# Kernel optimization log

Hardware: AMD Instinct MI355X
Metric: run time of the kernel (lower is better)

The kernel has to match this reference:

```python
import jax, jax.numpy as jnp
import numpy as np

B, D, N, L, M = 32, 64, 128, 192, 32  # batch, channels, nodes, seq_len, modes
LH = L // 2 + 1  # rfft length = 97


def setup_inputs() -> dict:
    key = jax.random.key(0)
    k1, k2, k3 = jax.random.split(key, 3)
    scale = 1.0 / (D * D)  # 1/(in_channels*out_channels)
    q = jax.random.normal(k1, (B, D, N, L), dtype=jnp.float32)
    w_real = scale * jax.random.uniform(k2, (N, D, D, M), dtype=jnp.float32)
    w_imag = scale * jax.random.uniform(k3, (N, D, D, M), dtype=jnp.float32)
    return {"q": q, "w_real": w_real, "w_imag": w_imag}


def reference(q, w_real, w_imag):
    # mode_select_method='lowest' -> index = [0, 1, ..., M-1] (static)
    index = np.arange(M)
    x = jnp.transpose(q, (0, 2, 1, 3))            # [B, N, D, L]
    x_ft = jnp.fft.rfft(x, axis=-1)               # [B, N, D, LH] complex64
    w = (w_real + 1j * w_imag).astype(jnp.complex64)  # [N, D, D, M]
    sel = x_ft[..., index]                        # gather selected modes [B, N, D, M]
    # fused replacement of the per-mode einsum loop: one batched complex einsum
    out_sel = jnp.einsum('bnim,niom->bnom', sel, w)  # [B, N, D, M]
    out_ft = jnp.zeros((B, N, D, LH), dtype=jnp.complex64).at[..., :M].set(out_sel)
    out = jnp.fft.irfft(out_ft, n=L, axis=-1)     # [B, N, D, L] real
    return jnp.transpose(out, (0, 2, 1, 3))       # [B, D, N, L]
```

## Files before the change

### kernel.cpp

```cpp
#include <hip/hip_runtime.h>
#include <stdint.h>


typedef __attribute__((ext_vector_type(8))) short short8;
typedef __attribute__((ext_vector_type(4))) float f32x4;
typedef __attribute__((ext_vector_type(4))) unsigned short u16x4;

__device__ __forceinline__ unsigned short f2bf(float f) {
  union { float fv; uint32_t u; } v; v.fv = f;
  uint32_t u = v.u;
  u += 0x7fffu + ((u >> 16) & 1u);
  return (unsigned short)(u >> 16);
}

__device__ __forceinline__ f32x4 zero4() { f32x4 z; z[0]=0.f; z[1]=0.f; z[2]=0.f; z[3]=0.f; return z; }

#define TWO_PI_OVER_L (6.283185307179586f / 192.0f)

__global__ __launch_bounds__(512, 1)
void k1d_dft(const float* __restrict__ q, unsigned short* __restrict__ Xp) {
  extern __shared__ char smem[];
  unsigned short* qB0 = (unsigned short*)smem;
  unsigned short* qB1 = (unsigned short*)(smem + 51200);
  unsigned short* Fb  = (unsigned short*)(smem + 102400);
  unsigned short* XE  = (unsigned short*)(smem + 128000);
  const int t = threadIdx.x, lane = t & 63, w = t >> 6;
  const int l15 = lane & 15, g = lane >> 4;
  const int bid = blockIdx.x;
  const int ih = bid & 1, bq = (bid >> 1) & 7, nq = bid >> 4;
  const int b0 = bq * 4;

  for (int idx = t; idx < 64 * 192; idx += 512) {
    int cat = idx / 192, l = idx - cat * 192;
    int m = cat >> 1;
    int r = (m * l) % 192;
    float ang = (float)r * TWO_PI_OVER_L;
    float v = (cat & 1) ? -__sinf(ang) : __cosf(ang);
    Fb[cat * 200 + l] = f2bf(v);
  }

  int srow[12], sqd[12];
#pragma unroll
  for (int j = 0; j < 12; ++j) {
    int fq = (w * 12 + j) * 64 + lane;
    srow[j] = fq / 48;
    sqd[j] = fq - srow[j] * 48;
  }
  size_t qoff[12];
#pragma unroll
  for (int j = 0; j < 12; ++j) {
    int row = srow[j];
    int b = b0 + (row >> 5), i = ih * 32 + (row & 31);
    qoff[j] = ((size_t)((b * 64 + i) * 128)) * 192 + sqd[j] * 4;
  }
  __syncthreads();

  float4 stg[12];
  {
    const int n = nq * 4;
#pragma unroll
    for (int j = 0; j < 12; ++j)
      stg[j] = *(const float4*)(q + qoff[j] + (size_t)n * 192);
#pragma unroll
    for (int j = 0; j < 12; ++j) {
      u16x4 h; h[0] = f2bf(stg[j].x); h[1] = f2bf(stg[j].y);
      h[2] = f2bf(stg[j].z); h[3] = f2bf(stg[j].w);
      *(u16x4*)(qB0 + srow[j] * 200 + sqd[j] * 4) = h;
    }
  }
  __syncthreads();

  for (int nn = 0; nn < 4; ++nn) {
    const int n = nq * 4 + nn;
    unsigned short* cur = (nn & 1) ? qB1 : qB0;
    unsigned short* nxt = (nn & 1) ? qB0 : qB1;

    if (nn < 3) {
#pragma unroll
      for (int j = 0; j < 12; ++j)
        stg[j] = *(const float4*)(q + qoff[j] + (size_t)(n + 1) * 192);
    }

    f32x4 acc[4];
#pragma unroll
    for (int a = 0; a < 4; ++a) acc[a] = zero4();
    const int row = w * 16 + l15;
#pragma unroll
    for (int kc = 0; kc < 6; ++kc) {
      short8 A = *(const short8*)(cur + row * 200 + kc * 32 + g * 8);
#pragma unroll
      for (int nt = 0; nt < 4; ++nt) {
        short8 Bf = *(const short8*)(Fb + (nt * 16 + l15) * 200 + kc * 32 + g * 8);
        acc[nt] = __builtin_amdgcn_mfma_f32_16x16x32_bf16(A, Bf, acc[nt], 0, 0, 0);
      }
    }

    if (nn < 3) {
#pragma unroll
      for (int j = 0; j < 12; ++j) {
        u16x4 h; h[0] = f2bf(stg[j].x); h[1] = f2bf(stg[j].y);
        h[2] = f2bf(stg[j].z); h[3] = f2bf(stg[j].w);
        *(u16x4*)(nxt + srow[j] * 200 + sqd[j] * 4) = h;
      }
    }
    __syncthreads();

    const int b_loc = w >> 1, i_base = (w & 1) * 16 + g * 4;
#pragma unroll
    for (int nt = 0; nt < 4; ++nt) {
      int cat = nt * 16 + l15;
      f32x4 v = acc[nt];
#pragma unroll
      for (int r = 0; r < 4; ++r)
        XE[cat * 132 + b_loc * 32 + i_base + r] = f2bf(v[r]);
    }
    __syncthreads();

#pragma unroll
    for (int cc2 = 0; cc2 < 2; ++cc2) {
      int ch = cc2 * 512 + t;
      int m = ch >> 5, c = (ch >> 4) & 1, g2 = (ch >> 2) & 3, dl = ch & 3;
      short8 v = *(const short8*)(XE + (2 * m + c) * 132 + dl * 32 + g2 * 8);
      int lanep = g2 * 16 + (b0 & 15) + dl;
      int off = n * 131072 + ((((m * 2 + c) * 2 + ih) * 2 + (b0 >> 4)) * 64 + lanep) * 8;
      *(short8*)(Xp + off) = v;
    }
  }
}

#define K2_OSTRIDE 34
#define K2_ISTRIDE 546
#define K2_CSTRIDE 34944
__global__ __launch_bounds__(512, 2)
void k2i_mix(const float* __restrict__ wr, const float* __restrict__ wi,
             const unsigned short* __restrict__ Xp, unsigned short* __restrict__ Yp) {
  extern __shared__ char smem[];
  unsigned short* T = (unsigned short*)smem;
  const int t = threadIdx.x, lane = t & 63, w = t >> 6;
  const int n = blockIdx.x >> 2, oq = blockIdx.x & 3;
  const int ol = lane & 15, il0 = (lane >> 4) * 8;

#pragma unroll
  for (int j = 0; j < 32; ++j) {
    int f = j * 512 + t;
    int mg = f & 7, o = (f >> 3) & 15, i = (f >> 7) & 63, c = (f >> 13) & 1;
    const float* src = (c ? wi : wr) + ((n * 64 + i) * 64 + oq * 16 + o) * 32 + mg * 4;
    float4 v = *(const float4*)src;
    u16x4 h; h[0] = f2bf(v.x); h[1] = f2bf(v.y); h[2] = f2bf(v.z); h[3] = f2bf(v.w);
    *(u16x4*)(T + c * K2_CSTRIDE + i * K2_ISTRIDE + o * K2_OSTRIDE + mg * 4) = h;
  }
  __syncthreads();

  unsigned short* yblk = Yp + (n * 4 + oq) * 32768;

#pragma unroll
  for (int mm = 0; mm < 4; ++mm) {
    int m = w * 4 + mm;
    f32x4 acc[2][2];
#pragma unroll
    for (int a = 0; a < 2; ++a)
#pragma unroll
      for (int b2 = 0; b2 < 2; ++b2) acc[a][b2] = zero4();

#pragma unroll
    for (int ic = 0; ic < 2; ++ic) {
      const unsigned short* xb = Xp + n * 131072 + m * 4096 + ic * 1024 + lane * 8;
      short8 Ar0 = *(const short8*)(xb);
      short8 Ar1 = *(const short8*)(xb + 512);
      short8 Ai0 = *(const short8*)(xb + 2048);
      short8 Ai1 = *(const short8*)(xb + 2048 + 512);

      const unsigned short* tb = T + (ic * 32 + il0) * K2_ISTRIDE + ol * K2_OSTRIDE + m;
      short8 Br, Bi, nBi;
#pragma unroll
      for (int e = 0; e < 8; ++e) {
        Br[e] = (short)tb[e * K2_ISTRIDE];
        Bi[e] = (short)tb[K2_CSTRIDE + e * K2_ISTRIDE];
        nBi[e] = Bi[e] ^ (short)0x8000;
      }

      acc[0][0] = __builtin_amdgcn_mfma_f32_16x16x32_bf16(Ar0, Br,  acc[0][0], 0, 0, 0);
      acc[0][0] = __builtin_amdgcn_mfma_f32_16x16x32_bf16(Ai0, nBi, acc[0][0], 0, 0, 0);
      acc[0][1] = __builtin_amdgcn_mfma_f32_16x16x32_bf16(Ar1, Br,  acc[0][1], 0, 0, 0);
      acc[0][1] = __builtin_amdgcn_mfma_f32_16x16x32_bf16(Ai1, nBi, acc[0][1], 0, 0, 0);
      acc[1][0] = __builtin_amdgcn_mfma_f32_16x16x32_bf16(Ar0, Bi,  acc[1][0], 0, 0, 0);
      acc[1][0] = __builtin_amdgcn_mfma_f32_16x16x32_bf16(Ai0, Br,  acc[1][0], 0, 0, 0);
      acc[1][1] = __builtin_amdgcn_mfma_f32_16x16x32_bf16(Ar1, Bi,  acc[1][1], 0, 0, 0);
      acc[1][1] = __builtin_amdgcn_mfma_f32_16x16x32_bf16(Ai1, Br,  acc[1][1], 0, 0, 0);
    }

    const int g = lane >> 4;
#pragma unroll
    for (int Mt = 0; Mt < 2; ++Mt)
#pragma unroll
      for (int r = 0; r < 4; ++r) {
        int b = Mt * 16 + g * 4 + r;
        unsigned short* yb = yblk + b * 1024 + (2 * m) * 16 + ol;
        yb[0]  = f2bf(acc[0][Mt][r]);
        yb[16] = f2bf(acc[1][Mt][r]);
      }
  }
}

__global__ __launch_bounds__(256, 4)
void k3_idft(const unsigned short* __restrict__ Yp, float* __restrict__ out) {
  extern __shared__ char smem[];
  unsigned short* Yl = (unsigned short*)smem;
  float* ol = (float*)(smem + 8448);
  const int t = threadIdx.x, lane = t & 63, w = t >> 6;
  const int n = blockIdx.x & 127, b = blockIdx.x >> 7;

  const unsigned short* ysrc = Yp + (n * 4 * 32 + b) * 1024;
#pragma unroll
  for (int j = 0; j < 2; ++j) {
    int f = j * 256 + t;
    int og = f & 1, cat = (f >> 1) & 63, oq = f >> 7;
    short8 v = *(const short8*)(ysrc + oq * 32768 + cat * 16 + og * 8);
    unsigned int* d = (unsigned int*)(Yl + cat * 66 + oq * 16 + og * 8);
    union { short8 s; unsigned int u[4]; } uu; uu.s = v;
    d[0] = uu.u[0]; d[1] = uu.u[1]; d[2] = uu.u[2]; d[3] = uu.u[3];
  }

  short8 Af[3][2];
#pragma unroll
  for (int jm = 0; jm < 3; ++jm) {
    int Mt = w + 4 * jm;
    int lt = Mt * 16 + (lane & 15);
#pragma unroll
    for (int kc = 0; kc < 2; ++kc) {
#pragma unroll
      for (int e = 0; e < 8; ++e) {
        int cat = kc * 32 + (lane >> 4) * 8 + e;
        int m = cat >> 1;
        int r = (m * lt) % 192;
        float ang = (float)r * TWO_PI_OVER_L;
        float coef = (m == 0) ? (1.0f / 192.0f) : (2.0f / 192.0f);
        float v = ((cat & 1) ? -__sinf(ang) : __cosf(ang)) * coef;
        Af[jm][kc][e] = (short)f2bf(v);
      }
    }
  }
  __syncthreads();

  f32x4 acc[3][4];
#pragma unroll
  for (int a = 0; a < 3; ++a)
#pragma unroll
    for (int bq = 0; bq < 4; ++bq) acc[a][bq] = zero4();

#pragma unroll
  for (int kc = 0; kc < 2; ++kc) {
    short8 Bf[4];
#pragma unroll
    for (int nt = 0; nt < 4; ++nt)
#pragma unroll
      for (int e = 0; e < 8; ++e) {
        int cat = kc * 32 + (lane >> 4) * 8 + e;
        Bf[nt][e] = (short)Yl[cat * 66 + nt * 16 + (lane & 15)];
      }
#pragma unroll
    for (int jm = 0; jm < 3; ++jm)
#pragma unroll
      for (int nt = 0; nt < 4; ++nt)
        acc[jm][nt] = __builtin_amdgcn_mfma_f32_16x16x32_bf16(Af[jm][kc], Bf[nt], acc[jm][nt], 0, 0, 0);
  }

#pragma unroll
  for (int jm = 0; jm < 3; ++jm) {
    int Mt = w + 4 * jm;
    int l0 = Mt * 16 + (lane >> 4) * 4;
#pragma unroll
    for (int nt = 0; nt < 4; ++nt) {
      int o = nt * 16 + (lane & 15);
      int lp = l0 ^ ((o & 7) << 2);
      *(f32x4*)(ol + o * 192 + lp) = acc[jm][nt];
    }
  }
  __syncthreads();

  float* dst = out + (b * 64 * 128 + n) * 192;
#pragma unroll
  for (int j = 0; j < 12; ++j) {
    int f = j * 256 + t;
    int o = f / 48, g2 = f - o * 48;
    int lp = g2 * 4;
    int l = lp ^ ((o & 7) << 2);
    f32x4 v = *(const f32x4*)(ol + o * 192 + lp);
    *(f32x4*)(dst + o * (128 * 192) + l) = v;
  }
}

extern "C" void kernel_launch(void* const* d_in, const int* in_sizes, int n_in,
                              void* d_out, int out_size, void* d_ws, size_t ws_size,
                              hipStream_t stream) {
  const float* q  = (const float*)d_in[0];
  const float* wr = (const float*)d_in[1];
  const float* wi = (const float*)d_in[2];
  float* out = (float*)d_out;

  unsigned short* Xp = (unsigned short*)d_ws;
  unsigned short* Yp = Xp + 16777216;

  hipFuncSetAttribute((const void*)k1d_dft, hipFuncAttributeMaxDynamicSharedMemorySize, 144896);
  hipFuncSetAttribute((const void*)k2i_mix, hipFuncAttributeMaxDynamicSharedMemorySize, 139776);
  hipFuncSetAttribute((const void*)k3_idft, hipFuncAttributeMaxDynamicSharedMemorySize, 57600);

  k1d_dft<<<dim3(512), dim3(512), 144896, stream>>>(q, Xp);
  k2i_mix<<<dim3(512), dim3(512), 139776, stream>>>(wr, wi, Xp, Yp);
  k3_idft<<<dim3(4096), dim3(256), 57600, stream>>>(Yp, out);
}
```

Baseline: 173.8 us.

## Split mix kernel over mode halves and hoist first q load before twiddle table build

The mixing kernel now splits each (node, output-quarter) block into two mode halves. That doubles the grid to 1024 blocks, halves the shared-memory weight tile, and raises launch bounds to allow more resident blocks per CU, aiming for better occupancy and latency hiding on the weight load. In the DFT kernel, the first slab of q is loaded into registers before the twiddle-table computation so the global load overlaps the sin/cos work. Each mix block still reads the full X tile for its modes, and register pressure in the DFT kernel rises slightly.

```diff
diff --git a/kernel.cpp b/kernel.cpp
--- a/kernel.cpp
+++ b/kernel.cpp
@@ -30,6 +30,28 @@
   const int ih = bid & 1, bq = (bid >> 1) & 7, nq = bid >> 4;
   const int b0 = bq * 4;
 
+  int srow[12], sqd[12];
+#pragma unroll
+  for (int j = 0; j < 12; ++j) {
+    int fq = (w * 12 + j) * 64 + lane;
+    srow[j] = fq / 48;
+    sqd[j] = fq - srow[j] * 48;
+  }
+  size_t qoff[12];
+#pragma unroll
+  for (int j = 0; j < 12; ++j) {
+    int row = srow[j];
+    int b = b0 + (row >> 5), i = ih * 32 + (row & 31);
+    qoff[j] = ((size_t)((b * 64 + i) * 128)) * 192 + sqd[j] * 4;
+  }
+  float4 stg[12];
+  {
+    const int n0 = nq * 4;
+#pragma unroll
+    for (int j = 0; j < 12; ++j)
+      stg[j] = *(const float4*)(q + qoff[j] + (size_t)n0 * 192);
+  }
+
   for (int idx = t; idx < 64 * 192; idx += 512) {
     int cat = idx / 192, l = idx - cat * 192;
     int m = cat >> 1;
@@ -39,34 +61,11 @@
     Fb[cat * 200 + l] = f2bf(v);
   }
 
-  int srow[12], sqd[12];
 #pragma unroll
   for (int j = 0; j < 12; ++j) {
-    int fq = (w * 12 + j) * 64 + lane;
-    srow[j] = fq / 48;
-    sqd[j] = fq - srow[j] * 48;
-  }
-  size_t qoff[12];
-#pragma unroll
-  for (int j = 0; j < 12; ++j) {
-    int row = srow[j];
-    int b = b0 + (row >> 5), i = ih * 32 + (row & 31);
-    qoff[j] = ((size_t)((b * 64 + i) * 128)) * 192 + sqd[j] * 4;
-  }
-  __syncthreads();
-
-  float4 stg[12];
-  {
-    const int n = nq * 4;
-#pragma unroll
-    for (int j = 0; j < 12; ++j)
-      stg[j] = *(const float4*)(q + qoff[j] + (size_t)n * 192);
-#pragma unroll
-    for (int j = 0; j < 12; ++j) {
-      u16x4 h; h[0] = f2bf(stg[j].x); h[1] = f2bf(stg[j].y);
-      h[2] = f2bf(stg[j].z); h[3] = f2bf(stg[j].w);
-      *(u16x4*)(qB0 + srow[j] * 200 + sqd[j] * 4) = h;
-    }
+    u16x4 h; h[0] = f2bf(stg[j].x); h[1] = f2bf(stg[j].y);
+    h[2] = f2bf(stg[j].z); h[3] = f2bf(stg[j].w);
+    *(u16x4*)(qB0 + srow[j] * 200 + sqd[j] * 4) = h;
   }
   __syncthreads();
 
@@ -128,34 +127,35 @@
   }
 }
 
-#define K2_OSTRIDE 34
-#define K2_ISTRIDE 546
-#define K2_CSTRIDE 34944
-__global__ __launch_bounds__(512, 2)
-void k2i_mix(const float* __restrict__ wr, const float* __restrict__ wi,
+#define M_OSTRIDE 18
+#define M_ISTRIDE 290
+#define M_CSTRIDE 18560
+__global__ __launch_bounds__(512, 4)
+void k2m_mix(const float* __restrict__ wr, const float* __restrict__ wi,
              const unsigned short* __restrict__ Xp, unsigned short* __restrict__ Yp) {
   extern __shared__ char smem[];
   unsigned short* T = (unsigned short*)smem;
   const int t = threadIdx.x, lane = t & 63, w = t >> 6;
-  const int n = blockIdx.x >> 2, oq = blockIdx.x & 3;
+  const int mh = blockIdx.x & 1, oq = (blockIdx.x >> 1) & 3, n = blockIdx.x >> 3;
   const int ol = lane & 15, il0 = (lane >> 4) * 8;
 
 #pragma unroll
-  for (int j = 0; j < 32; ++j) {
+  for (int j = 0; j < 16; ++j) {
     int f = j * 512 + t;
-    int mg = f & 7, o = (f >> 3) & 15, i = (f >> 7) & 63, c = (f >> 13) & 1;
-    const float* src = (c ? wi : wr) + ((n * 64 + i) * 64 + oq * 16 + o) * 32 + mg * 4;
+    int mg = f & 3, o = (f >> 2) & 15, i = (f >> 6) & 63, c = (f >> 12) & 1;
+    const float* src = (c ? wi : wr) + ((n * 64 + i) * 64 + oq * 16 + o) * 32 + mh * 16 + mg * 4;
     float4 v = *(const float4*)src;
     u16x4 h; h[0] = f2bf(v.x); h[1] = f2bf(v.y); h[2] = f2bf(v.z); h[3] = f2bf(v.w);
-    *(u16x4*)(T + c * K2_CSTRIDE + i * K2_ISTRIDE + o * K2_OSTRIDE + mg * 4) = h;
+    *(u16x4*)(T + c * M_CSTRIDE + i * M_ISTRIDE + o * M_OSTRIDE + mg * 4) = h;
   }
   __syncthreads();
 
   unsigned short* yblk = Yp + (n * 4 + oq) * 32768;
 
 #pragma unroll
-  for (int mm = 0; mm < 4; ++mm) {
-    int m = w * 4 + mm;
+  for (int mm = 0; mm < 2; ++mm) {
+    int m_loc = w * 2 + mm;
+    int m = mh * 16 + m_loc;
     f32x4 acc[2][2];
 #pragma unroll
     for (int a = 0; a < 2; ++a)
@@ -170,12 +170,12 @@
       short8 Ai0 = *(const short8*)(xb + 2048);
       short8 Ai1 = *(const short8*)(xb + 2048 + 512);
 
-      const unsigned short* tb = T + (ic * 32 + il0) * K2_ISTRIDE + ol * K2_OSTRIDE + m;
+      const unsigned short* tb = T + (ic * 32 + il0) * M_ISTRIDE + ol * M_OSTRIDE + m_loc;
       short8 Br, Bi, nBi;
 #pragma unroll
       for (int e = 0; e < 8; ++e) {
-        Br[e] = (short)tb[e * K2_ISTRIDE];
-        Bi[e] = (short)tb[K2_CSTRIDE + e * K2_ISTRIDE];
+        Br[e] = (short)tb[e * M_ISTRIDE];
+        Bi[e] = (short)tb[M_CSTRIDE + e * M_ISTRIDE];
         nBi[e] = Bi[e] ^ (short)0x8000;
       }
 
@@ -302,10 +302,10 @@
   unsigned short* Yp = Xp + 16777216;
 
   hipFuncSetAttribute((const void*)k1d_dft, hipFuncAttributeMaxDynamicSharedMemorySize, 144896);
-  hipFuncSetAttribute((const void*)k2i_mix, hipFuncAttributeMaxDynamicSharedMemorySize, 139776);
+  hipFuncSetAttribute((const void*)k2m_mix, hipFuncAttributeMaxDynamicSharedMemorySize, 74240);
   hipFuncSetAttribute((const void*)k3_idft, hipFuncAttributeMaxDynamicSharedMemorySize, 57600);
 
   k1d_dft<<<dim3(512), dim3(512), 144896, stream>>>(q, Xp);
-  k2i_mix<<<dim3(512), dim3(512), 139776, stream>>>(wr, wi, Xp, Yp);
+  k2m_mix<<<dim3(1024), dim3(512), 74240, stream>>>(wr, wi, Xp, Yp);
   k3_idft<<<dim3(4096), dim3(256), 57600, stream>>>(Yp, out);
 }
```

Result: slower. 179.4 us (+3.2%).

## Double-buffer DFT output staging, prefetch q early, and remap mix blocks

Applied to the files above, without the earlier changes.

The forward-DFT kernel now double-buffers its XE staging tile. The global store of node n-1's spectra overlaps the MFMA work for node n, which removes one __syncthreads per node iteration. The first q tile is loaded before the twiddle-table build so its latency is hidden, and the LDS row stride drops from 200 to 196 to change the bank mapping. The mix kernel remaps blockIdx so that consecutive blocks cover different nodes, likely to spread work across XCDs or memory channels. The cost is more LDS per block and a final drain step after the loop.

```diff
diff --git a/kernel.cpp b/kernel.cpp
--- a/kernel.cpp
+++ b/kernel.cpp
@@ -18,17 +18,40 @@
 #define TWO_PI_OVER_L (6.283185307179586f / 192.0f)
 
 __global__ __launch_bounds__(512, 1)
-void k1d_dft(const float* __restrict__ q, unsigned short* __restrict__ Xp) {
+void k1e_dft(const float* __restrict__ q, unsigned short* __restrict__ Xp) {
   extern __shared__ char smem[];
   unsigned short* qB0 = (unsigned short*)smem;
-  unsigned short* qB1 = (unsigned short*)(smem + 51200);
-  unsigned short* Fb  = (unsigned short*)(smem + 102400);
-  unsigned short* XE  = (unsigned short*)(smem + 128000);
+  unsigned short* qB1 = (unsigned short*)(smem + 50176);
+  unsigned short* Fb  = (unsigned short*)(smem + 100352);
+  unsigned short* XE0 = (unsigned short*)(smem + 125440);
+  unsigned short* XE1 = (unsigned short*)(smem + 142336);
   const int t = threadIdx.x, lane = t & 63, w = t >> 6;
   const int l15 = lane & 15, g = lane >> 4;
   const int bid = blockIdx.x;
   const int ih = bid & 1, bq = (bid >> 1) & 7, nq = bid >> 4;
   const int b0 = bq * 4;
+
+  int srow[12], sqd[12];
+#pragma unroll
+  for (int j = 0; j < 12; ++j) {
+    int fq = (w * 12 + j) * 64 + lane;
+    srow[j] = fq / 48;
+    sqd[j] = fq - srow[j] * 48;
+  }
+  size_t qoff[12];
+#pragma unroll
+  for (int j = 0; j < 12; ++j) {
+    int row = srow[j];
+    int b = b0 + (row >> 5), i = ih * 32 + (row & 31);
+    qoff[j] = ((size_t)((b * 64 + i) * 128)) * 192 + sqd[j] * 4;
+  }
+  float4 stg[12];
+  {
+    const int n0 = nq * 4;
+#pragma unroll
+    for (int j = 0; j < 12; ++j)
+      stg[j] = *(const float4*)(q + qoff[j] + (size_t)n0 * 192);
+  }
 
   for (int idx = t; idx < 64 * 192; idx += 512) {
     int cat = idx / 192, l = idx - cat * 192;
@@ -36,37 +59,14 @@
     int r = (m * l) % 192;
     float ang = (float)r * TWO_PI_OVER_L;
     float v = (cat & 1) ? -__sinf(ang) : __cosf(ang);
-    Fb[cat * 200 + l] = f2bf(v);
-  }
-
-  int srow[12], sqd[12];
+    Fb[cat * 196 + l] = f2bf(v);
+  }
+
 #pragma unroll
   for (int j = 0; j < 12; ++j) {
-    int fq = (w * 12 + j) * 64 + lane;
-    srow[j] = fq / 48;
-    sqd[j] = fq - srow[j] * 48;
-  }
-  size_t qoff[12];
-#pragma unroll
-  for (int j = 0; j < 12; ++j) {
-    int row = srow[j];
-    int b = b0 + (row >> 5), i = ih * 32 + (row & 31);
-    qoff[j] = ((size_t)((b * 64 + i) * 128)) * 192 + sqd[j] * 4;
-  }
-  __syncthreads();
-
-  float4 stg[12];
-  {
-    const int n = nq * 4;
-#pragma unroll
-    for (int j = 0; j < 12; ++j)
-      stg[j] = *(const float4*)(q + qoff[j] + (size_t)n * 192);
-#pragma unroll
-    for (int j = 0; j < 12; ++j) {
-      u16x4 h; h[0] = f2bf(stg[j].x); h[1] = f2bf(stg[j].y);
-      h[2] = f2bf(stg[j].z); h[3] = f2bf(stg[j].w);
-      *(u16x4*)(qB0 + srow[j] * 200 + sqd[j] * 4) = h;
-    }
+    u16x4 h; h[0] = f2bf(stg[j].x); h[1] = f2bf(stg[j].y);
+    h[2] = f2bf(stg[j].z); h[3] = f2bf(stg[j].w);
+    *(u16x4*)(qB0 + srow[j] * 196 + sqd[j] * 4) = h;
   }
   __syncthreads();
 
@@ -74,6 +74,8 @@
     const int n = nq * 4 + nn;
     unsigned short* cur = (nn & 1) ? qB1 : qB0;
     unsigned short* nxt = (nn & 1) ? qB0 : qB1;
+    unsigned short* XEc = (nn & 1) ? XE1 : XE0;
+    unsigned short* XEp = (nn & 1) ? XE0 : XE1;
 
     if (nn < 3) {
 #pragma unroll
@@ -81,18 +83,41 @@
         stg[j] = *(const float4*)(q + qoff[j] + (size_t)(n + 1) * 192);
     }
 
+    if (nn > 0) {
+      const int np = n - 1;
+#pragma unroll
+      for (int cc2 = 0; cc2 < 2; ++cc2) {
+        int ch = cc2 * 512 + t;
+        int m = ch >> 5, c = (ch >> 4) & 1, g2 = (ch >> 2) & 3, dl = ch & 3;
+        short8 v = *(const short8*)(XEp + (2 * m + c) * 132 + dl * 32 + g2 * 8);
+        int lanep = g2 * 16 + (b0 & 15) + dl;
+        int off = np * 131072 + ((((m * 2 + c) * 2 + ih) * 2 + (b0 >> 4)) * 64 + lanep) * 8;
+        *(short8*)(Xp + off) = v;
+      }
+    }
+
     f32x4 acc[4];
 #pragma unroll
     for (int a = 0; a < 4; ++a) acc[a] = zero4();
     const int row = w * 16 + l15;
 #pragma unroll
     for (int kc = 0; kc < 6; ++kc) {
-      short8 A = *(const short8*)(cur + row * 200 + kc * 32 + g * 8);
+      short8 A = *(const short8*)(cur + row * 196 + kc * 32 + g * 8);
 #pragma unroll
       for (int nt = 0; nt < 4; ++nt) {
-        short8 Bf = *(const short8*)(Fb + (nt * 16 + l15) * 200 + kc * 32 + g * 8);
+        short8 Bf = *(const short8*)(Fb + (nt * 16 + l15) * 196 + kc * 32 + g * 8);
         acc[nt] = __builtin_amdgcn_mfma_f32_16x16x32_bf16(A, Bf, acc[nt], 0, 0, 0);
       }
+    }
+
+    const int b_loc = w >> 1, i_base = (w & 1) * 16 + g * 4;
+#pragma unroll
+    for (int nt = 0; nt < 4; ++nt) {
+      int cat = nt * 16 + l15;
+      f32x4 v = acc[nt];
+#pragma unroll
+      for (int r = 0; r < 4; ++r)
+        XEc[cat * 132 + b_loc * 32 + i_base + r] = f2bf(v[r]);
     }
 
     if (nn < 3) {
@@ -100,29 +125,22 @@
       for (int j = 0; j < 12; ++j) {
         u16x4 h; h[0] = f2bf(stg[j].x); h[1] = f2bf(stg[j].y);
         h[2] = f2bf(stg[j].z); h[3] = f2bf(stg[j].w);
-        *(u16x4*)(nxt + srow[j] * 200 + sqd[j] * 4) = h;
-      }
-    }
+        *(u16x4*)(nxt + srow[j] * 196 + sqd[j] * 4) = h;
+      }
+    }
+
     __syncthreads();
-
-    const int b_loc = w >> 1, i_base = (w & 1) * 16 + g * 4;
-#pragma unroll
-    for (int nt = 0; nt < 4; ++nt) {
-      int cat = nt * 16 + l15;
-      f32x4 v = acc[nt];
-#pragma unroll
-      for (int r = 0; r < 4; ++r)
-        XE[cat * 132 + b_loc * 32 + i_base + r] = f2bf(v[r]);
-    }
-    __syncthreads();
-
+  }
+
+  {
+    const int np = nq * 4 + 3;
 #pragma unroll
     for (int cc2 = 0; cc2 < 2; ++cc2) {
       int ch = cc2 * 512 + t;
       int m = ch >> 5, c = (ch >> 4) & 1, g2 = (ch >> 2) & 3, dl = ch & 3;
-      short8 v = *(const short8*)(XE + (2 * m + c) * 132 + dl * 32 + g2 * 8);
+      short8 v = *(const short8*)(XE1 + (2 * m + c) * 132 + dl * 32 + g2 * 8);
       int lanep = g2 * 16 + (b0 & 15) + dl;
-      int off = n * 131072 + ((((m * 2 + c) * 2 + ih) * 2 + (b0 >> 4)) * 64 + lanep) * 8;
+      int off = np * 131072 + ((((m * 2 + c) * 2 + ih) * 2 + (b0 >> 4)) * 64 + lanep) * 8;
       *(short8*)(Xp + off) = v;
     }
   }
@@ -132,12 +150,13 @@
 #define K2_ISTRIDE 546
 #define K2_CSTRIDE 34944
 __global__ __launch_bounds__(512, 2)
-void k2i_mix(const float* __restrict__ wr, const float* __restrict__ wi,
+void k2s_mix(const float* __restrict__ wr, const float* __restrict__ wi,
              const unsigned short* __restrict__ Xp, unsigned short* __restrict__ Yp) {
   extern __shared__ char smem[];
   unsigned short* T = (unsigned short*)smem;
   const int t = threadIdx.x, lane = t & 63, w = t >> 6;
-  const int n = blockIdx.x >> 2, oq = blockIdx.x & 3;
+  const int d = blockIdx.x;
+  const int n = (d & 7) * 16 + (d >> 5), oq = (d >> 3) & 3;
   const int ol = lane & 15, il0 = (lane >> 4) * 8;
 
 #pragma unroll
@@ -301,11 +320,11 @@
   unsigned short* Xp = (unsigned short*)d_ws;
   unsigned short* Yp = Xp + 16777216;
 
-  hipFuncSetAttribute((const void*)k1d_dft, hipFuncAttributeMaxDynamicSharedMemorySize, 144896);
-  hipFuncSetAttribute((const void*)k2i_mix, hipFuncAttributeMaxDynamicSharedMemorySize, 139776);
+  hipFuncSetAttribute((const void*)k1e_dft, hipFuncAttributeMaxDynamicSharedMemorySize, 159232);
+  hipFuncSetAttribute((const void*)k2s_mix, hipFuncAttributeMaxDynamicSharedMemorySize, 139776);
   hipFuncSetAttribute((const void*)k3_idft, hipFuncAttributeMaxDynamicSharedMemorySize, 57600);
 
-  k1d_dft<<<dim3(512), dim3(512), 144896, stream>>>(q, Xp);
-  k2i_mix<<<dim3(512), dim3(512), 139776, stream>>>(wr, wi, Xp, Yp);
+  k1e_dft<<<dim3(512), dim3(512), 159232, stream>>>(q, Xp);
+  k2s_mix<<<dim3(512), dim3(512), 139776, stream>>>(wr, wi, Xp, Yp);
   k3_idft<<<dim3(4096), dim3(256), 57600, stream>>>(Yp, out);
 }
```

New measurement: 180.0 us. +3.6%, slower.
